# Kernel optimization log

Measured on AMD Instinct MI355X. Metric: run time of the kernel, lower is better.

Reference implementation:

```python
import jax, jax.numpy as jnp
import numpy as np

A, K, CIN, H, W = 8, 50, 64, 100, 352
C1, C2, C3, COUT = 128, 128, 256, 256


def setup_inputs() -> dict:
    key = jax.random.key(0)
    ks = jax.random.split(key, 16)

    def mkw(k, o, i, kh, kw):
        k1, k2 = jax.random.split(k)
        scale = (2.0 / (i * kh * kw)) ** 0.5 * 0.5  # damped He init to keep 8-layer relu stack stable
        return (jax.random.normal(k1, (o, i, kh, kw), jnp.float32) * scale,
                jax.random.normal(k2, (o,), jnp.float32) * 0.01)

    w1a, b1a = mkw(ks[0], C1, CIN, 3, 3)
    w1b, b1b = mkw(ks[1], C1, C1, 3, 3)
    w2a, b2a = mkw(ks[2], C2, C1, 3, 3)
    w2b, b2b = mkw(ks[3], C2, C2, 3, 3)
    w3a, b3a = mkw(ks[4], C3, C2, 3, 3)
    w3b, b3b = mkw(ks[5], C3, C3, 3, 3)
    wDa, bDa = mkw(ks[6], C3, C3, 3, 3)
    wDb, bDb = mkw(ks[7], COUT, C3, 1, 1)
    wF, bF = mkw(ks[8], COUT, COUT, 1, 1)

    feature = jax.random.normal(ks[9], (A, CIN, H, W), jnp.float32)

    # integer BEV boxes (left, right, up, down), right>left, down>up, vehicle-scale extents
    l = jax.random.randint(ks[10], (A, K), 0, W - 17)
    bw = jax.random.randint(ks[11], (A, K), 4, 17)
    u = jax.random.randint(ks[12], (A, K), 0, H - 17)
    bh = jax.random.randint(ks[13], (A, K), 4, 17)
    boxes = jnp.stack([l, l + bw, u, u + bh], axis=-1).astype(jnp.int32)  # [A,K,4]

    return dict(feature=feature, boxes=boxes,
                w1a=w1a, b1a=b1a, w1b=w1b, b1b=b1b,
                w2a=w2a, b2a=b2a, w2b=w2b, b2b=b2b,
                w3a=w3a, b3a=b3a, w3b=w3b, b3b=b3b,
                wDa=wDa, bDa=bDa, wDb=wDb, bDb=bDb,
                wF=wF, bF=bF)


def _conv(x, w, b, pad):
    y = jax.lax.conv_general_dilated(x, w, (1, 1), [(pad, pad), (pad, pad)],
                                     dimension_numbers=('NCHW', 'OIHW', 'NCHW'))
    return y + b[None, :, None, None]


def _superbox(feature, boxes, w1a, b1a, w1b, b1b, w2a, b2a, w2b, b2b,
              w3a, b3a, w3b, b3b, wDa, bDa, wDb, bDb, wF, bF):
    x = feature
    for (wi, bi) in ((w1a, b1a), (w1b, b1b), (w2a, b2a), (w2b, b2b),
                     (w3a, b3a), (w3b, b3b), (wDa, bDa)):
        x = jax.nn.relu(_conv(x, wi, bi, 1))
    x = jax.nn.relu(_conv(x, wDb, bDb, 0))        # [A,256,H,W] features_matching

    # get_box_feature: pool(relu(finalconv(crop))). finalconv is 1x1 (pointwise),
    # so this equals the box-mean of relu(finalconv(full map)) -> integral image.
    y = jax.nn.relu(_conv(x, wF, bF, 0))          # [A,256,H,W]
    S = jnp.pad(jnp.cumsum(jnp.cumsum(y, axis=2), axis=3),
                ((0, 0), (0, 0), (1, 0), (1, 0)))  # [A,256,H+1,W+1] integral image

    l, r, u, d = boxes[..., 0], boxes[..., 1], boxes[..., 2], boxes[..., 3]  # each [A,K]

    def agent_pool(Sa, la, ra, ua, da):
        # Sa: [C,H+1,W+1]; adjacent advanced indices -> [C,K]
        tot = Sa[:, da, ra] - Sa[:, ua, ra] - Sa[:, da, la] + Sa[:, ua, la]
        area = ((da - ua) * (ra - la)).astype(Sa.dtype)
        return (tot / area).T                     # [K,C]

    desc = jax.vmap(agent_pool)(S, l, r, u, d)    # [A,K,256]
    return desc


def reference(feature, boxes, w1a, b1a, w1b, b1b, w2a, b2a, w2b, b2b,
              w3a, b3a, w3b, b3b, wDa, bDa, wDb, bDb, wF, bF):
    return _superbox(feature, boxes, w1a, b1a, w1b, b1b, w2a, b2a, w2b, b2b,
                     w3a, b3a, w3b, b3b, wDa, bDa, wDb, bDb, wF, bF)
```

## Files before the change

kernel.cpp:

```cpp
#include <hip/hip_runtime.h>
#include <hip/hip_bf16.h>

typedef unsigned int u32;
typedef unsigned short u16;
typedef __attribute__((ext_vector_type(8))) short bf16x8;
typedef __attribute__((ext_vector_type(4))) float f32x4;

#define DEVI __device__ __forceinline__

constexpr int AG = 8, H = 100, W = 352, HP = 102, WP = 354;
constexpr int HWp = H * W;
constexpr int NB = 2 * WP + 2 * H;

DEVI u16 f2bf(float f) {
  __hip_bfloat16 h = __float2bfloat16(f);
  return *reinterpret_cast<u16*>(&h);
}
DEVI float bf2f(u16 v) { return __uint_as_float(((u32)v) << 16); }

DEVI int chperm(int j) { int v = j >> 3, r = j & 7; return (r < 4) ? 4 * v + r : 16 + 4 * v + (r - 4); }
DEVI int chlog(int c) { return (c & ~31) + chperm(c & 31); }

typedef __attribute__((address_space(1))) const u32 as1c_u32;
typedef __attribute__((address_space(3))) u32 as3_u32;
DEVI void gload16(const u16* g, u16* l) {
  __builtin_amdgcn_global_load_lds((as1c_u32*)(const void*)g, (as3_u32*)(void*)l, 16, 0, 0);
}

template <int N> DEVI void waitcnt_vm() {
  if constexpr (N == 0) asm volatile("s_waitcnt vmcnt(0)" ::: "memory");
  else if constexpr (N == 3) asm volatile("s_waitcnt vmcnt(3)" ::: "memory");
  else if constexpr (N == 4) asm volatile("s_waitcnt vmcnt(4)" ::: "memory");
  else asm volatile("s_waitcnt vmcnt(0)" ::: "memory");
}

constexpr int WL_MAXCH[7] = {7, 6, 5, 4, 4, 3, 2};
__global__ void build_wl(const int* __restrict__ boxes, int nbox,
                         int* __restrict__ wl) {
  __shared__ int cnt[7][512];
  __shared__ int base_l[8];
  int t = threadIdx.x;
  if (t == 0) {
    int b = 0;
    for (int l = 0; l < 7; ++l) { base_l[l] = b; b += nbox * WL_MAXCH[l]; }
    base_l[7] = b;
  }
  __syncthreads();
  int total = base_l[7];
  for (int i = t; i < total; i += 512) wl[i] = -1;
  if (t < nbox) {
    const int* bx = boxes + t * 4;
    int bw = bx[1] - bx[0], bh = bx[3] - bx[2];
#pragma unroll
    for (int l = 0; l < 4; ++l) {
      int halo = 6 - l;
      int cl = max(bx[0] - halo, 0), cr = min(bx[1] + halo, W);
      int r0 = max(bx[2] - halo, 0), r1 = min(bx[3] + halo, H);
      cnt[l][t] = min(((cr - cl) * (r1 - r0) + 127) >> 7, WL_MAXCH[l]);
    }
    cnt[4][t] = min(((bw + 4) * (bh + 4) + 127) >> 7, 4);
    cnt[5][t] = min(((bw + 2) * (bh + 2) + 127) >> 7, 3);
    cnt[6][t] = min((bw * bh + 127) >> 7, 2);
  }
  __syncthreads();
  if (t == 0) {
    for (int l = 0; l < 7; ++l) {
      int run = 0;
      for (int b = 0; b < nbox; ++b) {
        int c = cnt[l][b];
        cnt[l][b] = run;
        run += c;
      }
    }
  }
  __syncthreads();
  if (t < nbox) {
    const int* bx = boxes + t * 4;
    int bw = bx[1] - bx[0], bh = bx[3] - bx[2];
    int nc[7];
#pragma unroll
    for (int l = 0; l < 4; ++l) {
      int halo = 6 - l;
      int cl = max(bx[0] - halo, 0), cr = min(bx[1] + halo, W);
      int r0 = max(bx[2] - halo, 0), r1 = min(bx[3] + halo, H);
      nc[l] = min(((cr - cl) * (r1 - r0) + 127) >> 7, WL_MAXCH[l]);
    }
    nc[4] = min(((bw + 4) * (bh + 4) + 127) >> 7, 4);
    nc[5] = min(((bw + 2) * (bh + 2) + 127) >> 7, 3);
    nc[6] = min((bw * bh + 127) >> 7, 2);
#pragma unroll
    for (int l = 0; l < 7; ++l)
      for (int c = 0; c < nc[l]; ++c)
        wl[base_l[l] + cnt[l][t] + c] = (t << 4) | c;
  }
}

__global__ void convert_feat(const float* __restrict__ f, u16* __restrict__ dst) {
  __shared__ float t32[64][33];
  int blk = blockIdx.x;
  int wseg = blk % 11;
  int rest = blk / 11;
  int h = rest % H;
  int a = rest / H;
  int t = threadIdx.x;
  int wbase = wseg * 32;
  {
    int w = t & 31;
    int c0 = (t >> 5) * 8;
#pragma unroll
    for (int i = 0; i < 8; ++i) {
      int lc = c0 + i;
      t32[lc][w] = f[((size_t)(a * 64 + lc) * H + h) * W + wbase + w];
    }
  }
  __syncthreads();
  int p = t >> 3;
  int cs = (t & 7) * 8;
  u16 tmp[8];
#pragma unroll
  for (int j = 0; j < 8; ++j) {
    int c = cs + j;
    int lc = (c & 32) + chperm(c & 31);
    tmp[j] = f2bf(t32[lc][p]);
  }
  size_t ob = ((size_t)(a * HP + h + 1) * WP + (wbase + p + 1)) * 64 + cs;
  *reinterpret_cast<uint4*>(dst + ob) = *reinterpret_cast<uint4*>(tmp);
}

template <int C>
__global__ void zero_border(u16* __restrict__ buf, int nA) {
  constexpr int CH = C / 8;
  int idx = blockIdx.x * 256 + threadIdx.x;
  int pix = idx / CH;
  int cc = (idx - pix * CH) * 8;
  if (pix >= nA * NB) return;
  int a = pix / NB;
  int b = pix - a * NB;
  int h, w;
  if (b < WP) { h = 0; w = b; }
  else if (b < 2 * WP) { h = HP - 1; w = b - WP; }
  else {
    int bb = b - 2 * WP;
    int bb2 = (bb < H) ? bb : bb - H;
    h = 1 + bb2;
    w = (bb < H) ? 0 : (WP - 1);
  }
  size_t off = ((size_t)(a * HP + h) * WP + w) * C + cc;
  *reinterpret_cast<uint4*>(buf + off) = make_uint4(0u, 0u, 0u, 0u);
}

__global__ void repack_w(const float* __restrict__ w, u16* __restrict__ rp,
                         int O, int I, int taps) {
  int idx = blockIdx.x * 256 + threadIdx.x;
  int total = O * I * taps;
  if (idx >= total) return;
  int jj = idx & 7;
  int u = (idx >> 3) & 7;
  int r = (idx >> 6) % O;
  int s = idx / (O * 64);
  int KB = I >> 6;
  int kb = s % KB;
  int t = s / KB;
  int lu = u ^ (r & 7);
  int g = lu & 3, j32 = lu >> 2;
  int cp = (jj < 4) ? 4 * g + jj : 16 + 4 * g + (jj - 4);
  int i = kb * 64 + j32 * 32 + cp;
  int o = (r & ~31) + chperm(r & 31);
  rp[idx] = f2bf(w[((size_t)o * I + i) * taps + t]);
}

__global__ void repack_plain(const float* __restrict__ w, u16* __restrict__ rp) {
  int idx = blockIdx.x * 256 + threadIdx.x;
  int jj = idx & 7;
  int g = (idx >> 3) & 3;
  int r = (idx >> 5) & 255;
  int kb = idx >> 13;
  int cp = (jj < 4) ? 4 * g + jj : 16 + 4 * g + (jj - 4);
  int i = kb * 32 + cp;
  int o = chlog(r);
  rp[idx] = f2bf(w[(size_t)o * 256 + i]);
}

template <int CIN, int COUT, int MAXCH, int HALO>
__global__ __launch_bounds__(256, 2) void conv_boxk(
    const u16* __restrict__ in, const u16* __restrict__ wrp,
    const float* __restrict__ bias, u16* __restrict__ out,
    const int* __restrict__ boxes, const int* __restrict__ wl, int wbase) {
  constexpr int BM = 128, BN = 128, BK = 64, TAPS = 9;
  constexpr int KB = CIN / BK;
  constexpr int KS = TAPS * KB;
  constexpr int NT = 256;
  constexpr int NC = COUT / BN;
  constexpr int ACH = 4, AH = 2, BH = 2, HALF = 4;
  constexpr int ASZ = BM * BK;
  constexpr int BSZ = BN * BK;
  __shared__ u16 smem[2 * (ASZ + BSZ)];

  const int blk = blockIdx.x;
  const int cb = blk % NC;
  const int item = wl[wbase + blk / NC];
  if (item < 0) return;
  const int box = item >> 4;
  const int c0 = item & 15;
  const int* bx = boxes + box * 4;
  const int a = box / 50;
  const int cl = max(bx[0] - HALO, 0);
  const int cr = min(bx[1] + HALO, W);
  const int r0 = max(bx[2] - HALO, 0);
  const int r1 = min(bx[3] + HALO, H);
  const int bw = cr - cl;
  const int npx = bw * (r1 - r0);

  const int tid = threadIdx.x;
  const int lane = tid & 63;
  const int wid = tid >> 6;
  const int wr = wid >> 1;
  const int wc = wid & 1;

  int aoff[ACH];
#pragma unroll
  for (int i = 0; i < ACH; ++i) {
    int c = tid + i * NT;
    int p = c >> 3, u = c & 7;
    int lu = u ^ (p & 7);
    int idx = c0 * 128 + p;
    if (idx >= npx) idx = npx - 1;
    int ph = r0 + idx / bw;
    int pw = cl + idx % bw;
    aoff[i] = ((a * HP + ph + 1) * WP + (pw + 1)) * CIN + lu * 8;
  }

  f32x4 acc[4][4];
#pragma unroll
  for (int m = 0; m < 4; ++m)
#pragma unroll
    for (int n = 0; n < 4; ++n) acc[m][n] = f32x4{0.f, 0.f, 0.f, 0.f};

  const int g = lane >> 4;
  const int arow = lane & 15;
  const int fk = arow & 7;

  auto stage = [&](int s, int h) {
    int par = s & 1;
    u16* Ad = smem + par * ASZ;
    u16* Bd = smem + 2 * ASZ + par * BSZ;
    int t = s / KB;
    int kb = s - t * KB;
    int doff = kb * BK + ((t / 3 - 1) * WP + (t % 3 - 1)) * CIN;
    const u16* wtile = wrp + (size_t)s * (COUT * BK) + cb * BSZ;
#pragma unroll
    for (int i = h * AH; i < h * AH + AH; ++i)
      gload16(in + aoff[i] + doff, Ad + (tid + i * NT) * 8);
#pragma unroll
    for (int i = h * BH; i < h * BH + BH; ++i)
      gload16(wtile + (tid + i * NT) * 8, Bd + (tid + i * NT) * 8);
  };

  stage(0, 0);
  stage(0, 1);

  for (int s = 0; s < KS; ++s) {
    int par = s & 1;
    const u16* Ab = smem + par * ASZ;
    const u16* Bb = smem + 2 * ASZ + par * BSZ;
    if (s + 1 < KS) {
      stage(s + 1, 0);
      waitcnt_vm<HALF>();
    } else {
      waitcnt_vm<0>();
    }
    __builtin_amdgcn_s_barrier();

#pragma unroll
    for (int j = 0; j < 2; ++j) {
      bf16x8 af[4], bfr[4];
#pragma unroll
      for (int m = 0; m < 4; ++m)
        af[m] = *reinterpret_cast<const bf16x8*>(
            Ab + (wr * 64 + m * 16 + arow) * 64 + (((j * 4 + g) ^ fk) << 3));
#pragma unroll
      for (int n = 0; n < 4; ++n)
        bfr[n] = *reinterpret_cast<const bf16x8*>(
            Bb + (wc * 64 + n * 16 + arow) * 64 + (((j * 4 + g) ^ fk) << 3));
      __builtin_amdgcn_s_setprio(1);
#pragma unroll
      for (int m = 0; m < 4; ++m)
#pragma unroll
        for (int n = 0; n < 4; ++n)
          acc[m][n] = __builtin_amdgcn_mfma_f32_16x16x32_bf16(af[m], bfr[n], acc[m][n], 0, 0, 0);
      __builtin_amdgcn_s_setprio(0);
      if (j == 0 && s + 1 < KS) stage(s + 1, 1);
    }
    __builtin_amdgcn_s_barrier();
  }

  __syncthreads();
  float bs[4];
#pragma unroll
  for (int n = 0; n < 4; ++n) bs[n] = bias[chlog(cb * BN + wc * 64 + n * 16 + arow)];
  u16* et = smem + wid * 2048;
#pragma unroll
  for (int pp = 0; pp < 2; ++pp) {
    if (pp) __syncthreads();
#pragma unroll
    for (int mm = 0; mm < 2; ++mm) {
      int m = pp * 2 + mm;
#pragma unroll
      for (int rg = 0; rg < 4; ++rg) {
        int row = mm * 16 + g * 4 + rg;
#pragma unroll
        for (int n = 0; n < 4; ++n) {
          int col = (n * 16 + arow) ^ (g << 4);
          et[row * 64 + col] = f2bf(fmaxf(acc[m][n][rg] + bs[n], 0.f));
        }
      }
    }
    __syncthreads();
#pragma unroll
    for (int jj = 0; jj < 4; ++jj) {
      int p = jj * 8 + (lane >> 3);
      int un = lane & 7;
      int su = un ^ (((p >> 2) & 3) << 1);
      uint4 qv = *reinterpret_cast<const uint4*>(et + p * 64 + su * 8);
      int idx = c0 * 128 + wr * 64 + pp * 32 + p;
      if (idx >= npx) idx = npx - 1;
      int ph = r0 + idx / bw;
      int pw = cl + idx % bw;
      size_t ob = ((size_t)(a * HP + ph + 1) * WP + (pw + 1)) * COUT +
                  cb * BN + wc * 64 + un * 8;
      *reinterpret_cast<uint4*>(out + ob) = qv;
    }
  }
}

template <int CIN, int EOUT, int MAXCH, int MODE>
__global__ __launch_bounds__(256, 2) void conv_tl(
    const u16* __restrict__ in, const u16* __restrict__ wrp,
    const float* __restrict__ bias, u16* __restrict__ out,
    const int* __restrict__ boxes, const int* __restrict__ wl, int wbase) {
  constexpr int BM = 128, BN = 128, BK = 64, TAPS = 9;
  constexpr int KB = CIN / BK;
  constexpr int KS = TAPS * KB;
  constexpr int NT = 256;
  constexpr int NC = 2;
  constexpr int COUT = 256;
  constexpr int ACH = 4, AH = 2, BH = 2, HALF = 4;
  constexpr int ASZ = BM * BK;
  constexpr int BSZ = BN * BK;
  constexpr int TSLOT = (MODE == 0) ? 400 : (MODE == 1) ? 324 : 256;
  constexpr int TIN_SLOT = (MODE == 1) ? 400 : (MODE == 2) ? 324 : 0;
  __shared__ u16 smem[2 * (ASZ + BSZ)];

  const int blk = blockIdx.x;
  const int cb = blk % NC;
  const int item = wl[wbase + blk / NC];
  if (item < 0) return;
  const int box = item >> 4;
  const int c0 = item & 15;
  const int* bx = boxes + box * 4;
  const int a = box / 50;
  const int bw = bx[1] - bx[0], bh = bx[3] - bx[2];
  const int bwO = bw + 2 * EOUT, bhO = bh + 2 * EOUT;
  const int NPX = bwO * bhO;
  const int org_r = bx[2] - EOUT, org_c = bx[0] - EOUT;
  const int bwIn = bw + 2 * (EOUT + 1);

  const int tid = threadIdx.x;
  const int lane = tid & 63;
  const int wid = tid >> 6;
  const int wr = wid >> 1;
  const int wc = wid & 1;

  const u16* src = (MODE == 0) ? in : in + (size_t)box * TIN_SLOT * CIN;

  int aoff[ACH];
#pragma unroll
  for (int i = 0; i < ACH; ++i) {
    int c = tid + i * NT;
    int p = c >> 3, u = c & 7;
    int lu = u ^ (p & 7);
    int idx = c0 * 128 + p;
    if (idx >= NPX) idx = NPX - 1;
    int r = idx / bwO, cc = idx - r * bwO;
    if (MODE == 0) {
      int mr = org_r + r, mc = org_c + cc;
      mr = min(max(mr, 0), H - 1);
      mc = min(max(mc, 0), W - 1);
      aoff[i] = ((a * HP + mr + 1) * WP + (mc + 1)) * CIN + lu * 8;
    } else {
      aoff[i] = ((r + 1) * bwIn + (cc + 1)) * CIN + lu * 8;
    }
  }

  f32x4 acc[4][4];
#pragma unroll
  for (int m = 0; m < 4; ++m)
#pragma unroll
    for (int n = 0; n < 4; ++n) acc[m][n] = f32x4{0.f, 0.f, 0.f, 0.f};

  const int g = lane >> 4;
  const int arow = lane & 15;
  const int fk = arow & 7;
  const int stride = (MODE == 0) ? WP : bwIn;

  auto stage = [&](int s, int h) {
    int par = s & 1;
    u16* Ad = smem + par * ASZ;
    u16* Bd = smem + 2 * ASZ + par * BSZ;
    int t = s / KB;
    int kb = s - t * KB;
    int doff = kb * BK + ((t / 3 - 1) * stride + (t % 3 - 1)) * CIN;
    const u16* wtile = wrp + (size_t)s * (COUT * BK) + cb * BSZ;
#pragma unroll
    for (int i = h * AH; i < h * AH + AH; ++i)
      gload16(src + aoff[i] + doff, Ad + (tid + i * NT) * 8);
#pragma unroll
    for (int i = h * BH; i < h * BH + BH; ++i)
      gload16(wtile + (tid + i * NT) * 8, Bd + (tid + i * NT) * 8);
  };

  stage(0, 0);
  stage(0, 1);

  for (int s = 0; s < KS; ++s) {
    int par = s & 1;
    const u16* Ab = smem + par * ASZ;
    const u16* Bb = smem + 2 * ASZ + par * BSZ;
    if (s + 1 < KS) {
      stage(s + 1, 0);
      waitcnt_vm<HALF>();
    } else {
      waitcnt_vm<0>();
    }
    __builtin_amdgcn_s_barrier();

#pragma unroll
    for (int j = 0; j < 2; ++j) {
      bf16x8 af[4], bfr[4];
#pragma unroll
      for (int m = 0; m < 4; ++m)
        af[m] = *reinterpret_cast<const bf16x8*>(
            Ab + (wr * 64 + m * 16 + arow) * 64 + (((j * 4 + g) ^ fk) << 3));
#pragma unroll
      for (int n = 0; n < 4; ++n)
        bfr[n] = *reinterpret_cast<const bf16x8*>(
            Bb + (wc * 64 + n * 16 + arow) * 64 + (((j * 4 + g) ^ fk) << 3));
      __builtin_amdgcn_s_setprio(1);
#pragma unroll
      for (int m = 0; m < 4; ++m)
#pragma unroll
        for (int n = 0; n < 4; ++n)
          acc[m][n] = __builtin_amdgcn_mfma_f32_16x16x32_bf16(af[m], bfr[n], acc[m][n], 0, 0, 0);
      __builtin_amdgcn_s_setprio(0);
      if (j == 0 && s + 1 < KS) stage(s + 1, 1);
    }
    __builtin_amdgcn_s_barrier();
  }

  __syncthreads();
  float bs[4];
#pragma unroll
  for (int n = 0; n < 4; ++n) bs[n] = bias[chlog(cb * BN + wc * 64 + n * 16 + arow)];
  u16* et = smem + wid * 2048;
#pragma unroll
  for (int pp = 0; pp < 2; ++pp) {
    if (pp) __syncthreads();
#pragma unroll
    for (int mm = 0; mm < 2; ++mm) {
      int m = pp * 2 + mm;
#pragma unroll
      for (int rg = 0; rg < 4; ++rg) {
        int row = mm * 16 + g * 4 + rg;
#pragma unroll
        for (int n = 0; n < 4; ++n) {
          int col = (n * 16 + arow) ^ (g << 4);
          et[row * 64 + col] = f2bf(fmaxf(acc[m][n][rg] + bs[n], 0.f));
        }
      }
    }
    __syncthreads();
#pragma unroll
    for (int jj = 0; jj < 4; ++jj) {
      int p = jj * 8 + (lane >> 3);
      int un = lane & 7;
      int su = un ^ (((p >> 2) & 3) << 1);
      uint4 qv = *reinterpret_cast<const uint4*>(et + p * 64 + su * 8);
      int idx = c0 * 128 + wr * 64 + pp * 32 + p;
      if (idx >= NPX) idx = NPX - 1;
      if (MODE != 2) {
        int r2 = idx / bwO, c2 = idx - (idx / bwO) * bwO;
        int mr = org_r + r2, mc = org_c + c2;
        if (mr < 0 || mr >= H || mc < 0 || mc >= W)
          qv = make_uint4(0u, 0u, 0u, 0u);
      }
      size_t ob = ((size_t)box * TSLOT + idx) * COUT + cb * BN + wc * 64 + un * 8;
      *reinterpret_cast<uint4*>(out + ob) = qv;
    }
  }
}

__global__ __launch_bounds__(256) void fuse_box(
    const u16* __restrict__ x, const u16* __restrict__ wDbp,
    const float* __restrict__ bDb, const u16* __restrict__ wFp,
    const float* __restrict__ bF, const int* __restrict__ boxes,
    float* __restrict__ desc) {
  __shared__ u16 xT[16 * 256];
  const int blk = blockIdx.x;
  const int* bx = boxes + blk * 4;
  const int bw = bx[1] - bx[0];
  const int npx = bw * (bx[3] - bx[2]);
  const int nch = (npx + 15) >> 4;
  const int tid = threadIdx.x;
  const int lane = tid & 63;
  const int wc = tid >> 6;
  const int g = lane >> 4;
  const int arow = lane & 15;

  float b1[4], b2[4];
#pragma unroll
  for (int nf = 0; nf < 4; ++nf) {
    int ch = wc * 64 + nf * 16 + arow;
    b1[nf] = bDb[chlog(ch)];
    b2[nf] = bF[chlog(ch)];
  }
  float sums[4] = {0.f, 0.f, 0.f, 0.f};

  for (int ci = 0; ci < nch; ++ci) {
    int idx = ci * 16 + arow;
    if (idx >= npx) idx = npx - 1;
    const u16* ap = x + ((size_t)blk * 256 + idx) * 256;
    f32x4 a1[4];
#pragma unroll
    for (int nf = 0; nf < 4; ++nf) a1[nf] = f32x4{0.f, 0.f, 0.f, 0.f};
#pragma unroll
    for (int kb = 0; kb < 8; ++kb) {
      bf16x8 af = *reinterpret_cast<const bf16x8*>(ap + kb * 32 + g * 8);
#pragma unroll
      for (int nf = 0; nf < 4; ++nf) {
        bf16x8 bf_ = *reinterpret_cast<const bf16x8*>(
            wDbp + (((size_t)kb * 256 + wc * 64 + nf * 16 + arow) * 4 + g) * 8);
        a1[nf] = __builtin_amdgcn_mfma_f32_16x16x32_bf16(af, bf_, a1[nf], 0, 0, 0);
      }
    }
    if (ci) __syncthreads();
#pragma unroll
    for (int nf = 0; nf < 4; ++nf)
#pragma unroll
      for (int rg = 0; rg < 4; ++rg) {
        int px = g * 4 + rg;
        int ch = wc * 64 + nf * 16 + arow;
        int siu = (ch >> 3) ^ (px & 7);
        xT[px * 256 + siu * 8 + (ch & 7)] = f2bf(fmaxf(a1[nf][rg] + b1[nf], 0.f));
      }
    __syncthreads();
    f32x4 a2[4];
#pragma unroll
    for (int nf = 0; nf < 4; ++nf) a2[nf] = f32x4{0.f, 0.f, 0.f, 0.f};
#pragma unroll
    for (int kb = 0; kb < 8; ++kb) {
      int iu = kb * 4 + g;
      bf16x8 af2 = *reinterpret_cast<const bf16x8*>(
          xT + arow * 256 + (iu ^ (arow & 7)) * 8);
#pragma unroll
      for (int nf = 0; nf < 4; ++nf) {
        bf16x8 bf_ = *reinterpret_cast<const bf16x8*>(
            wFp + (((size_t)kb * 256 + wc * 64 + nf * 16 + arow) * 4 + g) * 8);
        a2[nf] = __builtin_amdgcn_mfma_f32_16x16x32_bf16(af2, bf_, a2[nf], 0, 0, 0);
      }
    }
#pragma unroll
    for (int nf = 0; nf < 4; ++nf)
#pragma unroll
      for (int rg = 0; rg < 4; ++rg) {
        int pidx = ci * 16 + g * 4 + rg;
        if (pidx < npx) sums[nf] += fmaxf(a2[nf][rg] + b2[nf], 0.f);
      }
  }
#pragma unroll
  for (int nf = 0; nf < 4; ++nf) {
    sums[nf] += __shfl_xor(sums[nf], 16, 64);
    sums[nf] += __shfl_xor(sums[nf], 32, 64);
  }
  if (g == 0) {
    float inv = 1.f / (float)npx;
#pragma unroll
    for (int nf = 0; nf < 4; ++nf) {
      int ch = wc * 64 + nf * 16 + arow;
      desc[(size_t)blk * 256 + chlog(ch)] = sums[nf] * inv;
    }
  }
}

extern "C" void kernel_launch(void* const* d_in, const int* in_sizes, int n_in,
                              void* d_out, int out_size, void* d_ws, size_t ws_size,
                              hipStream_t stream) {
  const float* feature = (const float*)d_in[0];
  const int* boxes = (const int*)d_in[1];
  const float* w1a = (const float*)d_in[2];
  const float* b1a = (const float*)d_in[3];
  const float* w1b = (const float*)d_in[4];
  const float* b1b = (const float*)d_in[5];
  const float* w2a = (const float*)d_in[6];
  const float* b2a = (const float*)d_in[7];
  const float* w2b = (const float*)d_in[8];
  const float* b2b = (const float*)d_in[9];
  const float* w3a = (const float*)d_in[10];
  const float* b3a = (const float*)d_in[11];
  const float* w3b = (const float*)d_in[12];
  const float* b3b = (const float*)d_in[13];
  const float* wDa = (const float*)d_in[14];
  const float* bDa = (const float*)d_in[15];
  const float* wDb = (const float*)d_in[16];
  const float* bDb = (const float*)d_in[17];
  const float* wF = (const float*)d_in[18];
  const float* bF = (const float*)d_in[19];

  const size_t e1a = (size_t)9 * 64 * 128;
  const size_t e128 = (size_t)9 * 128 * 128;
  const size_t e3a = (size_t)9 * 128 * 256;
  const size_t e256 = (size_t)9 * 256 * 256;
  const size_t ePl = (size_t)256 * 256;
  const size_t WELEMS = e1a + 3 * e128 + e3a + 2 * e256 + 2 * ePl;
  const size_t WB = WELEMS * 2 + (size_t)512 * 31 * 4;
  const size_t PER_A = (size_t)320 * HP * WP * 2;
  int aloc = (ws_size >= 8 * PER_A + WB) ? 8 : (ws_size >= 4 * PER_A + WB) ? 4 : 2;

  char* ws = (char*)d_ws;
  const size_t SZ64  = (size_t)aloc * HP * WP * 64 * 2;
  const size_t SZ128 = (size_t)aloc * HP * WP * 128 * 2;
  const size_t SZ192 = SZ64 + SZ128;
  u16* in64 = (u16*)(ws);
  u16* X    = (u16*)(ws + SZ64);
  u16* T0   = (u16*)(ws);
  u16* T2   = (u16*)(ws);
  u16* Y    = (u16*)(ws + SZ192);
  u16* T1   = (u16*)(ws + SZ192);
  u16* rp   = (u16*)(ws + SZ192 + SZ128);
  int* wl   = (int*)(ws + SZ192 + SZ128 + WELEMS * 2);

  const size_t o1a = 0;
  const size_t o1b = o1a + e1a;
  const size_t o2a = o1b + e128;
  const size_t o2b = o2a + e128;
  const size_t o3a = o2b + e128;
  const size_t o3b = o3a + e3a;
  const size_t oDa = o3b + e256;
  const size_t oDbP = oDa + e256;
  const size_t oFP = oDbP + ePl;

  auto rpk = [&](const float* wsrc, size_t off, int O, int I, int taps) {
    int total = O * I * taps;
    repack_w<<<(total + 255) / 256, 256, 0, stream>>>(wsrc, rp + off, O, I, taps);
  };
  rpk(w1a, o1a, 128, 64, 9);
  rpk(w1b, o1b, 128, 128, 9);
  rpk(w2a, o2a, 128, 128, 9);
  rpk(w2b, o2b, 128, 128, 9);
  rpk(w3a, o3a, 256, 128, 9);
  rpk(w3b, o3b, 256, 256, 9);
  rpk(wDa, oDa, 256, 256, 9);
  repack_plain<<<256, 256, 0, stream>>>(wDb, rp + oDbP);
  repack_plain<<<256, 256, 0, stream>>>(wF, rp + oFP);

  const int nbox = aloc * 50;
  int wb0 = 0;
  int wb1 = wb0 + nbox * 7;
  int wb2 = wb1 + nbox * 6;
  int wb3 = wb2 + nbox * 5;
  int wb4 = wb3 + nbox * 4;
  int wb5 = wb4 + nbox * 4;
  int wb6 = wb5 + nbox * 3;

  for (int a0 = 0; a0 < AG; a0 += aloc) {
    const int* bxs = boxes + (size_t)a0 * 50 * 4;
    build_wl<<<1, 512, 0, stream>>>(bxs, nbox, wl);
    zero_border<64><<<(aloc * NB * 8 + 255) / 256, 256, 0, stream>>>(in64, aloc);
    zero_border<128><<<(aloc * NB * 16 + 255) / 256, 256, 0, stream>>>(X, aloc);
    zero_border<128><<<(aloc * NB * 16 + 255) / 256, 256, 0, stream>>>(Y, aloc);

    convert_feat<<<aloc * H * 11, 256, 0, stream>>>(
        feature + (size_t)a0 * 64 * H * W, in64);

    conv_boxk<64, 128, 7, 6><<<nbox * 7, 256, 0, stream>>>(in64, rp + o1a, b1a, X, bxs, wl, wb0);
    conv_boxk<128, 128, 6, 5><<<nbox * 6, 256, 0, stream>>>(X, rp + o1b, b1b, Y, bxs, wl, wb1);
    conv_boxk<128, 128, 5, 4><<<nbox * 5, 256, 0, stream>>>(Y, rp + o2a, b2a, X, bxs, wl, wb2);
    conv_boxk<128, 128, 4, 3><<<nbox * 4, 256, 0, stream>>>(X, rp + o2b, b2b, Y, bxs, wl, wb3);
    conv_tl<128, 2, 4, 0><<<nbox * 4 * 2, 256, 0, stream>>>(Y, rp + o3a, b3a, T0, bxs, wl, wb4);
    conv_tl<256, 1, 3, 1><<<nbox * 3 * 2, 256, 0, stream>>>(T0, rp + o3b, b3b, T1, bxs, wl, wb5);
    conv_tl<256, 0, 2, 2><<<nbox * 2 * 2, 256, 0, stream>>>(T1, rp + oDa, bDa, T2, bxs, wl, wb6);
    fuse_box<<<nbox, 256, 0, stream>>>(
        T2, rp + oDbP, bDb, rp + oFP, bF, bxs,
        ((float*)d_out) + (size_t)a0 * 50 * 256);
  }
}
```

Measured before the change: 605.4 us.

## Interleave box work items across XCD slots and encode channel-block in item

The work-list builder now assigns each box to one of 8 interleaved slot groups with separate running offsets. It also expands the two output channel blocks into separate entries, so the conv kernels read cb from the item instead of blockIdx. The intent is to make real blocks dense and spread evenly across the GPU's XCDs instead of leaving blocks that exit early, improving load balance. This costs a larger work list, and the per-XCD counts can still be uneven.

```diff
diff --git a/kernel.cpp b/kernel.cpp
--- a/kernel.cpp
+++ b/kernel.cpp
@@ -35,14 +35,17 @@
 }
 
 constexpr int WL_MAXCH[7] = {7, 6, 5, 4, 4, 3, 2};
+constexpr int WL_NC[7] = {1, 1, 1, 1, 2, 2, 2};
 __global__ void build_wl(const int* __restrict__ boxes, int nbox,
                          int* __restrict__ wl) {
-  __shared__ int cnt[7][512];
+  __shared__ int ent[7][512];
+  __shared__ int pos[7][512];
   __shared__ int base_l[8];
   int t = threadIdx.x;
+  int nbox8 = (nbox + 7) & ~7;
   if (t == 0) {
     int b = 0;
-    for (int l = 0; l < 7; ++l) { base_l[l] = b; b += nbox * WL_MAXCH[l]; }
+    for (int l = 0; l < 7; ++l) { base_l[l] = b; b += nbox8 * WL_MAXCH[l] * WL_NC[l]; }
     base_l[7] = b;
   }
   __syncthreads();
@@ -56,20 +59,20 @@
       int halo = 6 - l;
       int cl = max(bx[0] - halo, 0), cr = min(bx[1] + halo, W);
       int r0 = max(bx[2] - halo, 0), r1 = min(bx[3] + halo, H);
-      cnt[l][t] = min(((cr - cl) * (r1 - r0) + 127) >> 7, WL_MAXCH[l]);
-    }
-    cnt[4][t] = min(((bw + 4) * (bh + 4) + 127) >> 7, 4);
-    cnt[5][t] = min(((bw + 2) * (bh + 2) + 127) >> 7, 3);
-    cnt[6][t] = min((bw * bh + 127) >> 7, 2);
+      ent[l][t] = min(((cr - cl) * (r1 - r0) + 127) >> 7, WL_MAXCH[l]);
+    }
+    ent[4][t] = min(((bw + 4) * (bh + 4) + 127) >> 7, 4) * 2;
+    ent[5][t] = min(((bw + 2) * (bh + 2) + 127) >> 7, 3) * 2;
+    ent[6][t] = min((bw * bh + 127) >> 7, 2) * 2;
   }
   __syncthreads();
   if (t == 0) {
     for (int l = 0; l < 7; ++l) {
-      int run = 0;
+      int run[8] = {0, 0, 0, 0, 0, 0, 0, 0};
       for (int b = 0; b < nbox; ++b) {
-        int c = cnt[l][b];
-        cnt[l][b] = run;
-        run += c;
+        int x = b & 7;
+        pos[l][b] = run[x];
+        run[x] += ent[l][b];
       }
     }
   }
@@ -88,10 +91,14 @@
     nc[4] = min(((bw + 4) * (bh + 4) + 127) >> 7, 4);
     nc[5] = min(((bw + 2) * (bh + 2) + 127) >> 7, 3);
     nc[6] = min((bw * bh + 127) >> 7, 2);
-#pragma unroll
-    for (int l = 0; l < 7; ++l)
+    int x = t & 7;
+#pragma unroll
+    for (int l = 0; l < 7; ++l) {
+      int off = pos[l][t];
       for (int c = 0; c < nc[l]; ++c)
-        wl[base_l[l] + cnt[l][t] + c] = (t << 4) | c;
+        for (int cbv = 0; cbv < WL_NC[l]; ++cbv)
+          wl[base_l[l] + x + 8 * (off++)] = (t << 6) | (c << 1) | cbv;
+    }
   }
 }
 
@@ -190,18 +197,16 @@
   constexpr int KB = CIN / BK;
   constexpr int KS = TAPS * KB;
   constexpr int NT = 256;
-  constexpr int NC = COUT / BN;
   constexpr int ACH = 4, AH = 2, BH = 2, HALF = 4;
   constexpr int ASZ = BM * BK;
   constexpr int BSZ = BN * BK;
   __shared__ u16 smem[2 * (ASZ + BSZ)];
 
-  const int blk = blockIdx.x;
-  const int cb = blk % NC;
-  const int item = wl[wbase + blk / NC];
+  const int item = wl[wbase + blockIdx.x];
   if (item < 0) return;
-  const int box = item >> 4;
-  const int c0 = item & 15;
+  const int box = item >> 6;
+  const int c0 = (item >> 1) & 31;
+  const int cb = item & 1;
   const int* bx = boxes + box * 4;
   const int a = box / 50;
   const int cl = max(bx[0] - HALO, 0);
@@ -342,7 +347,6 @@
   constexpr int KB = CIN / BK;
   constexpr int KS = TAPS * KB;
   constexpr int NT = 256;
-  constexpr int NC = 2;
   constexpr int COUT = 256;
   constexpr int ACH = 4, AH = 2, BH = 2, HALF = 4;
   constexpr int ASZ = BM * BK;
@@ -351,12 +355,11 @@
   constexpr int TIN_SLOT = (MODE == 1) ? 400 : (MODE == 2) ? 324 : 0;
   __shared__ u16 smem[2 * (ASZ + BSZ)];
 
-  const int blk = blockIdx.x;
-  const int cb = blk % NC;
-  const int item = wl[wbase + blk / NC];
+  const int item = wl[wbase + blockIdx.x];
   if (item < 0) return;
-  const int box = item >> 4;
-  const int c0 = item & 15;
+  const int box = item >> 6;
+  const int c0 = (item >> 1) & 31;
+  const int cb = item & 1;
   const int* bx = boxes + box * 4;
   const int a = box / 50;
   const int bw = bx[1] - bx[0], bh = bx[3] - bx[2];
@@ -621,7 +624,7 @@
   const size_t e256 = (size_t)9 * 256 * 256;
   const size_t ePl = (size_t)256 * 256;
   const size_t WELEMS = e1a + 3 * e128 + e3a + 2 * e256 + 2 * ePl;
-  const size_t WB = WELEMS * 2 + (size_t)512 * 31 * 4;
+  const size_t WB = WELEMS * 2 + (size_t)512 * 48 * 4;
   const size_t PER_A = (size_t)320 * HP * WP * 2;
   int aloc = (ws_size >= 8 * PER_A + WB) ? 8 : (ws_size >= 4 * PER_A + WB) ? 4 : 2;
 
@@ -663,13 +666,14 @@
   repack_plain<<<256, 256, 0, stream>>>(wF, rp + oFP);
 
   const int nbox = aloc * 50;
+  const int nbox8 = (nbox + 7) & ~7;
   int wb0 = 0;
-  int wb1 = wb0 + nbox * 7;
-  int wb2 = wb1 + nbox * 6;
-  int wb3 = wb2 + nbox * 5;
-  int wb4 = wb3 + nbox * 4;
-  int wb5 = wb4 + nbox * 4;
-  int wb6 = wb5 + nbox * 3;
+  int wb1 = wb0 + nbox8 * 7;
+  int wb2 = wb1 + nbox8 * 6;
+  int wb3 = wb2 + nbox8 * 5;
+  int wb4 = wb3 + nbox8 * 4;
+  int wb5 = wb4 + nbox8 * 8;
+  int wb6 = wb5 + nbox8 * 6;
 
   for (int a0 = 0; a0 < AG; a0 += aloc) {
     const int* bxs = boxes + (size_t)a0 * 50 * 4;
@@ -681,13 +685,13 @@
     convert_feat<<<aloc * H * 11, 256, 0, stream>>>(
         feature + (size_t)a0 * 64 * H * W, in64);
 
-    conv_boxk<64, 128, 7, 6><<<nbox * 7, 256, 0, stream>>>(in64, rp + o1a, b1a, X, bxs, wl, wb0);
-    conv_boxk<128, 128, 6, 5><<<nbox * 6, 256, 0, stream>>>(X, rp + o1b, b1b, Y, bxs, wl, wb1);
-    conv_boxk<128, 128, 5, 4><<<nbox * 5, 256, 0, stream>>>(Y, rp + o2a, b2a, X, bxs, wl, wb2);
-    conv_boxk<128, 128, 4, 3><<<nbox * 4, 256, 0, stream>>>(X, rp + o2b, b2b, Y, bxs, wl, wb3);
-    conv_tl<128, 2, 4, 0><<<nbox * 4 * 2, 256, 0, stream>>>(Y, rp + o3a, b3a, T0, bxs, wl, wb4);
-    conv_tl<256, 1, 3, 1><<<nbox * 3 * 2, 256, 0, stream>>>(T0, rp + o3b, b3b, T1, bxs, wl, wb5);
-    conv_tl<256, 0, 2, 2><<<nbox * 2 * 2, 256, 0, stream>>>(T1, rp + oDa, bDa, T2, bxs, wl, wb6);
+    conv_boxk<64, 128, 7, 6><<<nbox8 * 7, 256, 0, stream>>>(in64, rp + o1a, b1a, X, bxs, wl, wb0);
+    conv_boxk<128, 128, 6, 5><<<nbox8 * 6, 256, 0, stream>>>(X, rp + o1b, b1b, Y, bxs, wl, wb1);
+    conv_boxk<128, 128, 5, 4><<<nbox8 * 5, 256, 0, stream>>>(Y, rp + o2a, b2a, X, bxs, wl, wb2);
+    conv_boxk<128, 128, 4, 3><<<nbox8 * 4, 256, 0, stream>>>(X, rp + o2b, b2b, Y, bxs, wl, wb3);
+    conv_tl<128, 2, 4, 0><<<nbox8 * 8, 256, 0, stream>>>(Y, rp + o3a, b3a, T0, bxs, wl, wb4);
+    conv_tl<256, 1, 3, 1><<<nbox8 * 6, 256, 0, stream>>>(T0, rp + o3b, b3b, T1, bxs, wl, wb5);
+    conv_tl<256, 0, 2, 2><<<nbox8 * 4, 256, 0, stream>>>(T1, rp + oDa, bDa, T2, bxs, wl, wb6);
     fuse_box<<<nbox, 256, 0, stream>>>(
         T2, rp + oDbP, bDb, rp + oFP, bF, bxs,
         ((float*)d_out) + (size_t)a0 * 50 * 256);
```

After: 614.4 us. Within noise of the previous version (+1.5%).
